# Optimization experiments

Hardware: AMD Instinct MI355X
Metric: run time of the kernel (lower is better)

## Reference

```python
import jax, jax.numpy as jnp
import numpy as np

B = 262144
C = 128
NUM_CLASSES = 128   # fill_max for y
PAD = 2048
EPS = 1e-8
REJECT_THRESHOLD = 1


def setup_inputs() -> dict:
    key = jax.random.key(0)
    kx, ky = jax.random.split(key)
    x = jax.random.normal(kx, (B, C), dtype=jnp.float32)
    y = jax.random.randint(ky, (B,), 0, NUM_CLASSES)
    return {"x": x, "y": y}


def _decorrelate_loss(x, y):
    Bn, Cn = x.shape
    # per-class counts / sums (segment reduce replaces the python loop + boolean mask)
    counts = jax.ops.segment_sum(jnp.ones((Bn,), x.dtype), y, num_segments=NUM_CLASSES)  # [K]
    counts_i = counts.astype(jnp.int32)
    sums = jax.ops.segment_sum(x, y, num_segments=NUM_CLASSES)                            # [K, C]
    mean = sums / jnp.maximum(counts, 1.0)[:, None]
    centered = x - mean[y]                                                                # [B, C]
    # unbiased variance per class (torch .var default), guarded for count<=1
    var = jax.ops.segment_sum(centered * centered, y, num_segments=NUM_CLASSES) \
        / jnp.maximum(counts - 1.0, 1.0)[:, None]                                         # [K, C]
    xn = centered / jnp.sqrt(EPS + var)[y]                                                # [B, C]
    # sort rows by class so each class occupies a contiguous block, then slice fixed-size
    order = jnp.argsort(y)
    xs = jnp.concatenate([xn[order], jnp.zeros((PAD, Cn), x.dtype)], axis=0)              # [B+PAD, C]
    cum = jnp.cumsum(counts_i)
    starts = jnp.concatenate([jnp.zeros((1,), jnp.int32), cum[:-1]])                      # exclusive cumsum
    gathered = jax.vmap(lambda s: jax.lax.dynamic_slice(xs, (s, 0), (PAD, Cn)))(starts)   # [K, PAD, C]
    row_valid = (jnp.arange(PAD)[None, :] < counts_i[:, None]).astype(x.dtype)            # [K, PAD]
    g = gathered * row_valid[:, :, None]
    # per-class correlation matrices, all at once
    corr = jnp.einsum('kpc,kpd->kcd', g, g)                                               # [K, C, C]
    sq_sum = jnp.sum(corr * corr, axis=(1, 2))                                            # [K]
    diag_sq = jnp.sum(jnp.einsum('kcc->kc', corr) ** 2, axis=1)                           # [K]
    off_mean = (sq_sum - diag_sq) / (Cn * (Cn - 1))                                       # off_diagonal(.)^2 mean
    valid = counts_i > REJECT_THRESHOLD
    loss = jnp.sum(jnp.where(valid, off_mean, 0.0))
    n_count = jnp.sum(jnp.where(valid, counts, 0.0))
    return jnp.where(n_count > 0, loss / n_count, 0.0)


def reference(x, y):
    return _decorrelate_loss(x, y)
```

## Files before the change

kernel.cpp:

```cpp
#include <hip/hip_runtime.h>

#define B_ROWS   262144
#define C_DIM    128
#define K_CLS    128
#define PAD_R    2048
#define PAD2     4096
#define QSPLIT   4
#define QROWS    (PAD_R / QSPLIT)
#define TROWS    32
#define LSTRIDE  132
#define EPS_F    1e-8f
#define CHUNK    1024
#define G_CHUNKS 256

typedef float f32x4  __attribute__((ext_vector_type(4)));
typedef short bf16x8 __attribute__((ext_vector_type(8)));

__device__ __forceinline__ unsigned f2bf(float f) {
  unsigned u = __float_as_uint(f);
  return (u + 0x7fffu + ((u >> 16) & 1u)) >> 16;
}
__device__ __forceinline__ unsigned packbf(float a, float b) {
  return f2bf(a) | (f2bf(b) << 16);
}

__global__ __launch_bounds__(256) void hist_kernel(const int* __restrict__ y,
                                                   int* __restrict__ hist,
                                                   float* __restrict__ numden) {
  __shared__ int h[K_CLS];
  int g = blockIdx.x, tid = threadIdx.x;
  if (g == 0 && tid < 64) numden[tid] = 0.f;
  if (tid < K_CLS) h[tid] = 0;
  __syncthreads();
  for (int j = tid; j < CHUNK; j += 256) atomicAdd(&h[y[g * CHUNK + j]], 1);
  __syncthreads();
  if (tid < K_CLS) hist[g * K_CLS + tid] = h[tid];
}

__global__ __launch_bounds__(256) void scan_kernel(int* __restrict__ hist,
                                                   int* __restrict__ counts) {
  __shared__ int s[G_CHUNKS];
  int k = blockIdx.x, g = threadIdx.x;
  int v = hist[g * K_CLS + k];
  s[g] = v;
  __syncthreads();
  for (int off = 1; off < G_CHUNKS; off <<= 1) {
    int t = (g >= off) ? s[g - off] : 0;
    __syncthreads();
    s[g] += t;
    __syncthreads();
  }
  hist[g * K_CLS + k] = s[g] - v;
  if (g == G_CHUNKS - 1) counts[k] = s[g];
}

__global__ __launch_bounds__(256) void rank_kernel(const int* __restrict__ y,
                                                   const int* __restrict__ hist,
                                                   int* __restrict__ ord) {
  __shared__ unsigned short cnt_sub[16][K_CLS];
  __shared__ int offs[K_CLS];
  const int g = blockIdx.x, tid = threadIdx.x;
  const int lane = tid & 63, w = tid >> 6;
  if (tid < K_CLS) offs[tid] = hist[g * K_CLS + tid];
  {
    unsigned int* cz = (unsigned int*)cnt_sub;
    for (int i = tid; i < 16 * K_CLS / 2; i += 256) cz[i] = 0;
  }
  __syncthreads();

  int yv[4], rig[4];
  #pragma unroll
  for (int i = 0; i < 4; ++i) {
    const int s = w * 4 + i;
    const int yy = y[g * CHUNK + s * 64 + lane];
    unsigned long long m = ~0ULL;
    #pragma unroll
    for (int b = 0; b < 7; ++b) {
      unsigned long long bb = __ballot((yy >> b) & 1);
      m &= ((yy >> b) & 1) ? bb : ~bb;
    }
    const unsigned long long lt = (1ULL << lane) - 1ULL;
    rig[i] = (int)__popcll(m & lt);
    yv[i] = yy;
    const int leader = __ffsll((long long)m) - 1;
    if (lane == leader) cnt_sub[s][yy] = (unsigned short)__popcll(m);
  }
  __syncthreads();

  if (tid < K_CLS) {
    int run = 0;
    #pragma unroll
    for (int s = 0; s < 16; ++s) {
      int t = cnt_sub[s][tid];
      cnt_sub[s][tid] = (unsigned short)run;
      run += t;
    }
  }
  __syncthreads();

  #pragma unroll
  for (int i = 0; i < 4; ++i) {
    const int s = w * 4 + i;
    const int k = yv[i];
    const int R = offs[k] + (int)cnt_sub[s][k] + rig[i];
    if (R < PAD2) ord[k * PAD2 + R] = g * CHUNK + s * 64 + lane;
  }
}

__global__ __launch_bounds__(512, 4) void gemm_kernel(const float* __restrict__ x,
                                                      const int* __restrict__ ord,
                                                      const int* __restrict__ counts,
                                                      float* __restrict__ spart,
                                                      float* __restrict__ sums_part,
                                                      float* __restrict__ sqs_part,
                                                      float* __restrict__ ovfs_part) {
  __shared__ unsigned int lds[2 * (TROWS / 2) * LSTRIDE];
  __shared__ int ord_l[QROWS];
  const int blk = blockIdx.x;
  const int k = blk >> 2, quarter = blk & 3;
  const int cnt_full = counts[k];
  const int T = cnt_full < PAD_R ? cnt_full : PAD_R;
  const int r_base = quarter * QROWS;
  const int rend = (T < r_base + QROWS) ? T : (r_base + QROWS);
  const int nr = rend - r_base;
  const int nt = (nr > 0) ? ((nr + TROWS - 1) / TROWS) : 0;

  const int tid = threadIdx.x;
  const int lane = tid & 63;
  const int w = tid >> 6;
  const int wr = w >> 1, wc = w & 1;
  const int p = tid >> 5;
  const int lc = tid & 31;

  f32x4 acc[2][4];
  #pragma unroll
  for (int i = 0; i < 2; ++i)
    #pragma unroll
    for (int j = 0; j < 4; ++j) acc[i][j] = (f32x4){0.f, 0.f, 0.f, 0.f};
  float sum4[4] = {0.f, 0.f, 0.f, 0.f}, sq4[4] = {0.f, 0.f, 0.f, 0.f};

  const int* ordk = ord + k * PAD2;

  if (tid < QROWS) {
    int vi = ordk[r_base + tid];
    ord_l[tid] = ((unsigned)vi < B_ROWS) ? vi : 0;
  }
  __syncthreads();

  auto load_tile = [&](int t, f32x4* vv) {
    const int rr = t * TROWS + 2 * p;
    const int2 idx = *(const int2*)(&ord_l[rr]);
    const int rg = r_base + rr;
    const size_t co = (size_t)(lc << 2);
    const f32x4 z = (f32x4){0.f, 0.f, 0.f, 0.f};
    vv[0] = (rg + 0 < rend) ? *(const f32x4*)(x + (size_t)idx.x * C_DIM + co) : z;
    vv[1] = (rg + 1 < rend) ? *(const f32x4*)(x + (size_t)idx.y * C_DIM + co) : z;
  };

  auto write_tile = [&](unsigned int* buf, const f32x4* vv) {
    #pragma unroll
    for (int j = 0; j < 2; ++j)
      #pragma unroll
      for (int e = 0; e < 4; ++e) { float t = vv[j][e]; sum4[e] += t; sq4[e] += t * t; }
    uint4 pk;
    pk.x = packbf(vv[0][0], vv[1][0]);
    pk.y = packbf(vv[0][1], vv[1][1]);
    pk.z = packbf(vv[0][2], vv[1][2]);
    pk.w = packbf(vv[0][3], vv[1][3]);
    *(uint4*)(&buf[p * LSTRIDE + (lc << 2)]) = pk;
  };

  auto compute_tile = [&](const unsigned int* buf) {
    const int q2 = lane >> 4;
    const int fr = lane & 15;
    const unsigned int* base = buf + q2 * 4 * LSTRIDE;
    bf16x8 afr[2], bfr[4];
    #pragma unroll
    for (int mi = 0; mi < 2; ++mi) {
      const int c = wr * 32 + mi * 16 + fr;
      union { int4 i; bf16x8 h; } u;
      u.i.x = base[0 * LSTRIDE + c];
      u.i.y = base[1 * LSTRIDE + c];
      u.i.z = base[2 * LSTRIDE + c];
      u.i.w = base[3 * LSTRIDE + c];
      afr[mi] = u.h;
    }
    #pragma unroll
    for (int ni = 0; ni < 4; ++ni) {
      const int d = wc * 64 + ni * 16 + fr;
      union { int4 i; bf16x8 h; } u;
      u.i.x = base[0 * LSTRIDE + d];
      u.i.y = base[1 * LSTRIDE + d];
      u.i.z = base[2 * LSTRIDE + d];
      u.i.w = base[3 * LSTRIDE + d];
      bfr[ni] = u.h;
    }
    #pragma unroll
    for (int mi = 0; mi < 2; ++mi)
      #pragma unroll
      for (int ni = 0; ni < 4; ++ni)
        acc[mi][ni] = __builtin_amdgcn_mfma_f32_16x16x32_bf16(afr[mi], bfr[ni], acc[mi][ni], 0, 0, 0);
  };

  f32x4 va[2], vb[2];
  if (nt > 0) { load_tile(0, va); write_tile(lds, va); }
  if (nt > 1) load_tile(1, vb);
  __syncthreads();
  int cur = 0;
  const int BUFSZ = (TROWS / 2) * LSTRIDE;
  for (int t = 0; t < nt; t += 2) {
    if (t + 1 < nt) write_tile(lds + (unsigned)(cur ^ 1) * BUFSZ, vb);
    if (t + 2 < nt) load_tile(t + 2, va);
    compute_tile(lds + (unsigned)cur * BUFSZ);
    __syncthreads();
    cur ^= 1;
    if (t + 1 >= nt) break;
    if (t + 2 < nt) write_tile(lds + (unsigned)(cur ^ 1) * BUFSZ, va);
    if (t + 3 < nt) load_tile(t + 3, vb);
    compute_tile(lds + (unsigned)cur * BUFSZ);
    __syncthreads();
    cur ^= 1;
  }

  float osum[4] = {0.f, 0.f, 0.f, 0.f}, osq[4] = {0.f, 0.f, 0.f, 0.f};
  const int colo = lc << 2;
  for (int r = PAD_R + quarter + (p << 2); r < cnt_full; r += 64) {
    int row = ordk[r];
    f32x4 vv = *(const f32x4*)(x + (size_t)row * C_DIM + colo);
    #pragma unroll
    for (int e = 0; e < 4; ++e) { float t = vv[e]; osum[e] += t; osq[e] += t * t; }
  }

  __syncthreads();
  float* red = (float*)lds;
  if (tid < 3 * C_DIM) red[tid] = 0.f;
  __syncthreads();
  #pragma unroll
  for (int e = 0; e < 4; ++e) {
    atomicAdd(&red[colo + e], sum4[e]);
    atomicAdd(&red[C_DIM + colo + e], sq4[e] + osq[e]);
    atomicAdd(&red[2 * C_DIM + colo + e], osum[e]);
  }
  __syncthreads();
  if (tid < C_DIM) {
    sums_part[(quarter * K_CLS + k) * C_DIM + tid] = red[tid];
    sqs_part [(quarter * K_CLS + k) * C_DIM + tid] = red[C_DIM + tid];
    ovfs_part[(quarter * K_CLS + k) * C_DIM + tid] = red[2 * C_DIM + tid];
  }
  float* sp = spart + (size_t)(quarter * K_CLS + k) * (C_DIM * C_DIM);
  #pragma unroll
  for (int mi = 0; mi < 2; ++mi)
    #pragma unroll
    for (int ni = 0; ni < 4; ++ni)
      #pragma unroll
      for (int r = 0; r < 4; ++r) {
        int c = wr * 32 + mi * 16 + ((lane >> 4) << 2) + r;
        int d = wc * 64 + ni * 16 + (lane & 15);
        sp[c * C_DIM + d] = acc[mi][ni][r];
      }
}

__global__ __launch_bounds__(512) void finalize_kernel(const float* __restrict__ spart,
                                                       const float* __restrict__ sums_part,
                                                       const float* __restrict__ sqs_part,
                                                       const float* __restrict__ ovfs_part,
                                                       const int* __restrict__ counts,
                                                       float* __restrict__ numden) {
  __shared__ float m_l[C_DIM], is_l[C_DIM], st_l[C_DIM];
  __shared__ float wred[8];
  int k = blockIdx.x, tid = threadIdx.x;
  int count = counts[k];
  float Tf = (float)(count < PAD_R ? count : PAD_R);
  if (tid < C_DIM) {
    float s_tr = 0.f, osum = 0.f, fsq = 0.f;
    #pragma unroll
    for (int j = 0; j < QSPLIT; ++j) {
      s_tr += sums_part[(j * K_CLS + k) * C_DIM + tid];
      osum += ovfs_part[(j * K_CLS + k) * C_DIM + tid];
      fsq  += sqs_part [(j * K_CLS + k) * C_DIM + tid];
    }
    float fsum = s_tr + osum;
    float cf = (float)count;
    float m = fsum / fmaxf(cf, 1.f);
    float var = (fsq - cf * m * m) / fmaxf(cf - 1.f, 1.f);
    m_l[tid] = m;
    is_l[tid] = rsqrtf(var + EPS_F);
    st_l[tid] = s_tr;
  }
  __syncthreads();
  float local = 0.f;
  for (int e4 = tid * 4; e4 < C_DIM * C_DIM; e4 += 512 * 4) {
    int c = e4 >> 7, d0 = e4 & 127;
    f32x4 sa = (f32x4){0.f, 0.f, 0.f, 0.f};
    #pragma unroll
    for (int j = 0; j < QSPLIT; ++j) {
      f32x4 sj = *(const f32x4*)(spart + (size_t)(j * K_CLS + k) * (C_DIM * C_DIM) + e4);
      #pragma unroll
      for (int e = 0; e < 4; ++e) sa[e] += sj[e];
    }
    #pragma unroll
    for (int e = 0; e < 4; ++e) {
      int d = d0 + e;
      float corr = is_l[c] * is_l[d] *
                   (sa[e] - m_l[c] * st_l[d] - m_l[d] * st_l[c] + Tf * m_l[c] * m_l[d]);
      if (c != d) local += corr * corr;
    }
  }
  for (int off = 32; off > 0; off >>= 1) local += __shfl_down(local, off);
  int lane = tid & 63, wid = tid >> 6;
  if (lane == 0) wred[wid] = local;
  __syncthreads();
  if (tid == 0 && count > 1) {
    float tot = 0.f;
    #pragma unroll
    for (int i = 0; i < 8; ++i) tot += wred[i];
    atomicAdd(&numden[0], tot * (1.f / (float)(C_DIM * (C_DIM - 1))));
    atomicAdd(&numden[1], (float)count);
  }
}

__global__ void div_kernel(const float* __restrict__ numden, float* __restrict__ out) {
  if (threadIdx.x == 0 && blockIdx.x == 0)
    out[0] = numden[1] > 0.f ? numden[0] / numden[1] : 0.f;
}

extern "C" void kernel_launch(void* const* d_in, const int* in_sizes, int n_in,
                              void* d_out, int out_size, void* d_ws, size_t ws_size,
                              hipStream_t stream) {
  (void)in_sizes; (void)n_in; (void)out_size; (void)ws_size;
  const float* x = (const float*)d_in[0];
  const int*   y = (const int*)d_in[1];
  float* out = (float*)d_out;
  char* ws = (char*)d_ws;

  float* numden    = (float*)(ws + 0);
  int*   hist      = (int*)(ws + 256);
  int*   counts    = (int*)(ws + 131328);
  int*   ord       = (int*)(ws + 132096);
  float* sums_part = (float*)(ws + 2229248);
  float* sqs_part  = (float*)(ws + 2491392);
  float* ovfs_part = (float*)(ws + 2753536);
  float* spart     = (float*)(ws + 3015680);

  hist_kernel<<<G_CHUNKS, 256, 0, stream>>>(y, hist, numden);
  scan_kernel<<<K_CLS, 256, 0, stream>>>(hist, counts);
  rank_kernel<<<G_CHUNKS, 256, 0, stream>>>(y, hist, ord);
  gemm_kernel<<<QSPLIT * K_CLS, 512, 0, stream>>>(x, ord, counts, spart, sums_part,
                                                  sqs_part, ovfs_part);
  finalize_kernel<<<K_CLS, 512, 0, stream>>>(spart, sums_part, sqs_part, ovfs_part,
                                             counts, numden);
  div_kernel<<<1, 64, 0, stream>>>(numden, out);
}
```

Before: 71.12 us.

## Deepen global-load prefetch to two tiles and use LDS-only barrier waits

Restructures the double-buffered tile loop so global loads run two tiles ahead instead of one. Loads become unconditional, since ord_l holds a valid index for every row, and the row-validity masking moves into write_tile. Barriers now wait only on lgkmcnt before s_barrier instead of __syncthreads, so in-flight global loads are not drained at each barrier. The aim is to hide gather latency behind MFMA compute, at the cost of more live registers and some redundant loads for padding rows.

Result: no change. 71.12 us (+0.0%).

```diff
diff --git a/kernel.cpp b/kernel.cpp
--- a/kernel.cpp
+++ b/kernel.cpp
@@ -23,6 +23,12 @@
 __device__ __forceinline__ unsigned packbf(float a, float b) {
   return f2bf(a) | (f2bf(b) << 16);
 }
+
+#define TILE_BARRIER()                                      \
+  do {                                                      \
+    asm volatile("s_waitcnt lgkmcnt(0)" ::: "memory");      \
+    __builtin_amdgcn_s_barrier();                           \
+  } while (0)
 
 __global__ __launch_bounds__(256) void hist_kernel(const int* __restrict__ y,
                                                    int* __restrict__ hist,
@@ -150,23 +156,26 @@
   auto load_tile = [&](int t, f32x4* vv) {
     const int rr = t * TROWS + 2 * p;
     const int2 idx = *(const int2*)(&ord_l[rr]);
-    const int rg = r_base + rr;
     const size_t co = (size_t)(lc << 2);
+    vv[0] = *(const f32x4*)(x + (size_t)idx.x * C_DIM + co);
+    vv[1] = *(const f32x4*)(x + (size_t)idx.y * C_DIM + co);
+  };
+
+  auto write_tile = [&](unsigned int* buf, const f32x4* vv, int t) {
+    const int rg = r_base + t * TROWS + 2 * p;
     const f32x4 z = (f32x4){0.f, 0.f, 0.f, 0.f};
-    vv[0] = (rg + 0 < rend) ? *(const f32x4*)(x + (size_t)idx.x * C_DIM + co) : z;
-    vv[1] = (rg + 1 < rend) ? *(const f32x4*)(x + (size_t)idx.y * C_DIM + co) : z;
-  };
-
-  auto write_tile = [&](unsigned int* buf, const f32x4* vv) {
-    #pragma unroll
-    for (int j = 0; j < 2; ++j)
-      #pragma unroll
-      for (int e = 0; e < 4; ++e) { float t = vv[j][e]; sum4[e] += t; sq4[e] += t * t; }
+    const f32x4 w0 = (rg + 0 < rend) ? vv[0] : z;
+    const f32x4 w1 = (rg + 1 < rend) ? vv[1] : z;
+    #pragma unroll
+    for (int e = 0; e < 4; ++e) {
+      sum4[e] += w0[e] + w1[e];
+      sq4[e] += w0[e] * w0[e] + w1[e] * w1[e];
+    }
     uint4 pk;
-    pk.x = packbf(vv[0][0], vv[1][0]);
-    pk.y = packbf(vv[0][1], vv[1][1]);
-    pk.z = packbf(vv[0][2], vv[1][2]);
-    pk.w = packbf(vv[0][3], vv[1][3]);
+    pk.x = packbf(w0[0], w1[0]);
+    pk.y = packbf(w0[1], w1[1]);
+    pk.z = packbf(w0[2], w1[2]);
+    pk.w = packbf(w0[3], w1[3]);
     *(uint4*)(&buf[p * LSTRIDE + (lc << 2)]) = pk;
   };
 
@@ -202,24 +211,32 @@
         acc[mi][ni] = __builtin_amdgcn_mfma_f32_16x16x32_bf16(afr[mi], bfr[ni], acc[mi][ni], 0, 0, 0);
   };
 
-  f32x4 va[2], vb[2];
-  if (nt > 0) { load_tile(0, va); write_tile(lds, va); }
-  if (nt > 1) load_tile(1, vb);
-  __syncthreads();
-  int cur = 0;
   const int BUFSZ = (TROWS / 2) * LSTRIDE;
-  for (int t = 0; t < nt; t += 2) {
-    if (t + 1 < nt) write_tile(lds + (unsigned)(cur ^ 1) * BUFSZ, vb);
-    if (t + 2 < nt) load_tile(t + 2, va);
-    compute_tile(lds + (unsigned)cur * BUFSZ);
-    __syncthreads();
-    cur ^= 1;
-    if (t + 1 >= nt) break;
-    if (t + 2 < nt) write_tile(lds + (unsigned)(cur ^ 1) * BUFSZ, va);
-    if (t + 3 < nt) load_tile(t + 3, vb);
-    compute_tile(lds + (unsigned)cur * BUFSZ);
-    __syncthreads();
-    cur ^= 1;
+  if (nt > 0) {
+    f32x4 vA[2], vB[2];
+    load_tile(0, vA);
+    if (nt > 1) load_tile(1, vB);
+    write_tile(lds, vA, 0);
+    if (nt > 2) load_tile(2, vA);
+    TILE_BARRIER();
+    int cur = 0;
+    for (int t = 0; t < nt; t += 2) {
+      if (t + 1 < nt) {
+        write_tile(lds + (unsigned)(cur ^ 1) * BUFSZ, vB, t + 1);
+        if (t + 3 < nt) load_tile(t + 3, vB);
+      }
+      compute_tile(lds + (unsigned)cur * BUFSZ);
+      TILE_BARRIER();
+      cur ^= 1;
+      if (t + 1 >= nt) break;
+      if (t + 2 < nt) {
+        write_tile(lds + (unsigned)(cur ^ 1) * BUFSZ, vA, t + 2);
+        if (t + 4 < nt) load_tile(t + 4, vA);
+      }
+      compute_tile(lds + (unsigned)cur * BUFSZ);
+      TILE_BARRIER();
+      cur ^= 1;
+    }
   }
 
   float osum[4] = {0.f, 0.f, 0.f, 0.f}, osq[4] = {0.f, 0.f, 0.f, 0.f};
```
